# Optimization experiments

Hardware: AMD Instinct MI355X
Metric: run time of the kernel (lower is better)

## Reference

```python
import jax, jax.numpy as jnp
import numpy as np

NUM_HEADING_BIN = 12
NUM_SIZE_CLUSTER = 8
BS = 524288
# KITTI-style mean box sizes (l, w, h) for 8 size clusters
G_MEAN_SIZE_ARR = np.array([
    [3.88, 1.63, 1.53], [0.84, 0.66, 1.76], [1.76, 0.60, 1.74], [16.17, 2.58, 3.23],
    [3.90, 1.60, 1.56], [1.73, 0.58, 1.37], [0.91, 0.48, 1.78], [2.06, 1.86, 1.66]],
    dtype=np.float32)


def setup_inputs() -> dict:
    key = jax.random.key(0)
    ks = jax.random.split(key, 13)
    f = lambda k, s: jax.random.normal(k, s, dtype=jnp.float32)
    return {
        "center": f(ks[0], (BS, 3)),
        "center_label": f(ks[1], (BS, 3)),
        "stage1_center": f(ks[2], (BS, 3)),
        "heading_scores": f(ks[3], (BS, 12)),
        "heading_residuals_normalized": f(ks[4], (BS, 12)),
        "heading_residuals": f(ks[5], (BS, 12)),
        "heading_class_label": jax.random.randint(ks[6], (BS,), 0, 12, dtype=jnp.int64),
        "heading_residuals_label": f(ks[7], (BS,)),
        "size_scores": f(ks[8], (BS, 8)),
        "size_residuals_normalized": f(ks[9], (BS, 8, 3)),
        "size_residuals": f(ks[10], (BS, 8, 3)),
        "size_class_label": jax.random.randint(ks[11], (BS,), 0, 8, dtype=jnp.int64),
        "size_residuals_label": f(ks[12], (BS, 3)),
    }


def _huber(err, delta):
    a = jnp.abs(err)
    q = jnp.minimum(a, delta)
    return jnp.mean(0.5 * q * q + delta * (a - q))


_SX = jnp.array([1, 1, -1, -1, 1, 1, -1, -1], dtype=jnp.float32)
_SY = jnp.array([1, 1, 1, 1, -1, -1, -1, -1], dtype=jnp.float32)
_SZ = jnp.array([1, -1, -1, 1, 1, -1, -1, 1], dtype=jnp.float32)


def _corners3d(centers, headings, sizes):
    # centers (bs,3), headings (bs,), sizes (bs,3) [l,w,h] -> (bs,8,3)
    l, w, h = sizes[:, 0:1], sizes[:, 1:2], sizes[:, 2:3]
    x = 0.5 * l * _SX  # (bs,8)
    y = 0.5 * h * _SY
    z = 0.5 * w * _SZ
    c = jnp.cos(headings)[:, None]
    s = jnp.sin(headings)[:, None]
    xr = c * x + s * z   # rotation about y-axis
    zr = -s * x + c * z
    return jnp.stack([xr, y, zr], axis=-1) + centers[:, None, :]


def reference(center, center_label, stage1_center, heading_scores,
              heading_residuals_normalized, heading_residuals, heading_class_label,
              heading_residuals_label, size_scores, size_residuals_normalized,
              size_residuals, size_class_label, size_residuals_label):
    corner_loss_weight, box_loss_weight = 10.0, 1.0
    mean_sizes = jnp.asarray(G_MEAN_SIZE_ARR)  # (8,3)
    hcls = heading_class_label.astype(jnp.int32)
    scls = size_class_label.astype(jnp.int32)

    center_loss = _huber(jnp.linalg.norm(center - center_label, axis=1), 2.0)
    stage1_center_loss = _huber(jnp.linalg.norm(center - stage1_center, axis=1), 1.0)

    h_logp = jax.nn.log_softmax(heading_scores, axis=1)
    heading_class_loss = -jnp.mean(jnp.take_along_axis(h_logp, hcls[:, None], axis=1))
    s_logp = jax.nn.log_softmax(size_scores, axis=1)
    size_class_loss = -jnp.mean(jnp.take_along_axis(s_logp, scls[:, None], axis=1))

    # heading residual loss (one-hot sum == gather at class index)
    hres_label_norm = heading_residuals_label / (np.pi / NUM_HEADING_BIN)
    hres_pred = jnp.take_along_axis(heading_residuals_normalized, hcls[:, None], axis=1)[:, 0]
    heading_res_loss = _huber(hres_pred - hres_label_norm, 1.0)

    # size residual loss
    sres_pred = jnp.take_along_axis(size_residuals_normalized, scls[:, None, None], axis=1)[:, 0]  # (bs,3)
    mean_size_label = mean_sizes[scls]  # (bs,3)
    sres_label_norm = size_residuals_label / mean_size_label
    size_res_loss = _huber(jnp.linalg.norm(sres_label_norm - sres_pred, axis=1), 1.0)

    # corner loss: gt_mask one-hot sum over (NH,NS) grid == gather (hcls, scls) box
    bin_centers = jnp.arange(NUM_HEADING_BIN, dtype=jnp.float32) * (2.0 * np.pi / NUM_HEADING_BIN)
    heading_pred = jnp.take_along_axis(heading_residuals, hcls[:, None], axis=1)[:, 0] + bin_centers[hcls]
    size_pred = mean_size_label + jnp.take_along_axis(size_residuals, scls[:, None, None], axis=1)[:, 0]
    corners_pred = _corners3d(center, heading_pred, size_pred)  # (bs,8,3)

    heading_label = heading_residuals_label + bin_centers[hcls]
    size_label = mean_size_label + size_residuals_label
    corners_gt = _corners3d(center_label, heading_label, size_label)
    corners_gt_flip = _corners3d(center_label, heading_label + np.pi, size_label)
    corners_dist = jnp.minimum(jnp.linalg.norm(corners_pred - corners_gt, axis=-1),
                               jnp.linalg.norm(corners_pred - corners_gt_flip, axis=-1))
    corners_loss = _huber(corners_dist, 1.0)

    total_loss = box_loss_weight * (center_loss + heading_class_loss + size_class_loss
                                    + heading_res_loss * 20.0 + size_res_loss * 20.0
                                    + stage1_center_loss + corner_loss_weight * corners_loss)
    return total_loss
```

## Files before the change

kernel.cpp:

```cpp
#include <hip/hip_runtime.h>
#include <math.h>


constexpr int BS_N = 524288;
constexpr int NBLK = 4096;

__constant__ float G_MEAN[8][3] = {
    {3.88f, 1.63f, 1.53f}, {0.84f, 0.66f, 1.76f}, {1.76f, 0.60f, 1.74f},
    {16.17f, 2.58f, 3.23f}, {3.90f, 1.60f, 1.56f}, {1.73f, 0.58f, 1.37f},
    {0.91f, 0.48f, 1.78f}, {2.06f, 1.86f, 1.66f}
};
__constant__ float G_RCP[8][3] = {
    {1.0f/3.88f, 1.0f/1.63f, 1.0f/1.53f}, {1.0f/0.84f, 1.0f/0.66f, 1.0f/1.76f},
    {1.0f/1.76f, 1.0f/0.60f, 1.0f/1.74f}, {1.0f/16.17f, 1.0f/2.58f, 1.0f/3.23f},
    {1.0f/3.90f, 1.0f/1.60f, 1.0f/1.56f}, {1.0f/1.73f, 1.0f/0.58f, 1.0f/1.37f},
    {1.0f/0.91f, 1.0f/0.48f, 1.0f/1.78f}, {1.0f/2.06f, 1.0f/1.86f, 1.0f/1.66f}
};

__device__ __forceinline__ float huber_pos(float a, float delta) {
    return (a <= delta) ? 0.5f * a * a : delta * (a - 0.5f * delta);
}
__device__ __forceinline__ float huber_norm2(float d2, float delta) {
    return (d2 <= delta * delta) ? 0.5f * d2
                                 : delta * (sqrtf(d2) - 0.5f * delta);
}
__device__ __forceinline__ float sel4(float4 v, int k) {
    float r = v.x;
    r = (k == 1) ? v.y : r;
    r = (k == 2) ? v.z : r;
    r = (k == 3) ? v.w : r;
    return r;
}
__device__ __forceinline__ float sel12(float4 a, float4 b, float4 c, int k) {
    float r = sel4(a, k);
    r = (k >= 4) ? sel4(b, k - 4) : r;
    r = (k >= 8) ? sel4(c, k - 8) : r;
    return r;
}
__device__ __forceinline__ float sel8(float4 a, float4 b, int k) {
    float r = sel4(a, k);
    r = (k >= 4) ? sel4(b, k - 4) : r;
    return r;
}
__device__ __forceinline__ void sel_row3(
    float4 a, float4 b, float4 c, float4 d, float4 e, float4 f, int s,
    float &o0, float &o1, float &o2)
{
    const float r[24] = {a.x,a.y,a.z,a.w, b.x,b.y,b.z,b.w, c.x,c.y,c.z,c.w,
                         d.x,d.y,d.z,d.w, e.x,e.y,e.z,e.w, f.x,f.y,f.z,f.w};
    o0 = r[0]; o1 = r[1]; o2 = r[2];
    #pragma unroll
    for (int k = 1; k < 8; ++k) {
        const bool m = (s == k);
        o0 = m ? r[3*k+0] : o0;
        o1 = m ? r[3*k+1] : o1;
        o2 = m ? r[3*k+2] : o2;
    }
}

__global__ __launch_bounds__(128) void bbox_partial(
    const float* __restrict__ center,
    const float* __restrict__ center_label,
    const float* __restrict__ stage1_center,
    const float* __restrict__ heading_scores,
    const float* __restrict__ hrn,
    const float* __restrict__ hres,
    const int*   __restrict__ hcls_in,
    const float* __restrict__ hres_label,
    const float* __restrict__ size_scores,
    const float* __restrict__ srn,
    const float* __restrict__ sres,
    const int*   __restrict__ scls_in,
    const float* __restrict__ sres_label,
    float* __restrict__ block_out)
{
    const int i = blockIdx.x * 128 + threadIdx.x;

    const int h = hcls_in[i];
    const int s = scls_in[i];

    const float cx = center[3*i+0], cy = center[3*i+1], cz = center[3*i+2];
    const float lx = center_label[3*i+0], ly = center_label[3*i+1], lz = center_label[3*i+2];
    const float tx = stage1_center[3*i+0], ty = stage1_center[3*i+1], tz = stage1_center[3*i+2];
    const float sl0 = sres_label[3*i+0], sl1 = sres_label[3*i+1], sl2 = sres_label[3*i+2];
    const float hrl = hres_label[i];

    const float4* hsp = reinterpret_cast<const float4*>(heading_scores + 12*i);
    const float4 hsA = hsp[0], hsB = hsp[1], hsC = hsp[2];
    const float4* ssp = reinterpret_cast<const float4*>(size_scores + 8*i);
    const float4 ssA = ssp[0], ssB = ssp[1];

    const float4* hnp = reinterpret_cast<const float4*>(hrn + 12*i);
    const float4 hn0 = hnp[0], hn1 = hnp[1], hn2 = hnp[2];
    const float4* hep = reinterpret_cast<const float4*>(hres + 12*i);
    const float4 he0 = hep[0], he1 = hep[1], he2 = hep[2];

    const float4* snp = reinterpret_cast<const float4*>(srn + 24*i);
    const float4 sn0 = snp[0], sn1 = snp[1], sn2 = snp[2],
                 sn3 = snp[3], sn4 = snp[4], sn5 = snp[5];
    const float4* srp = reinterpret_cast<const float4*>(sres + 24*i);
    const float4 sr0 = srp[0], sr1 = srp[1], sr2 = srp[2],
                 sr3 = srp[3], sr4 = srp[4], sr5 = srp[5];

    float contrib = 0.0f;

    const float dx0 = cx - lx, dy0 = cy - ly, dz0 = cz - lz;
    contrib += huber_norm2(dx0*dx0 + dy0*dy0 + dz0*dz0, 2.0f);
    {
        const float ax = cx - tx, ay = cy - ty, az = cz - tz;
        contrib += huber_norm2(ax*ax + ay*ay + az*az, 1.0f);
    }

    {
        float m = fmaxf(fmaxf(fmaxf(hsA.x,hsA.y),fmaxf(hsA.z,hsA.w)),
                  fmaxf(fmaxf(fmaxf(hsB.x,hsB.y),fmaxf(hsB.z,hsB.w)),
                        fmaxf(fmaxf(hsC.x,hsC.y),fmaxf(hsC.z,hsC.w))));
        float se = __expf(hsA.x-m)+__expf(hsA.y-m)+__expf(hsA.z-m)+__expf(hsA.w-m)
                 + __expf(hsB.x-m)+__expf(hsB.y-m)+__expf(hsB.z-m)+__expf(hsB.w-m)
                 + __expf(hsC.x-m)+__expf(hsC.y-m)+__expf(hsC.z-m)+__expf(hsC.w-m);
        contrib += m + __logf(se) - sel12(hsA, hsB, hsC, h);
    }
    {
        float m = fmaxf(fmaxf(fmaxf(ssA.x,ssA.y),fmaxf(ssA.z,ssA.w)),
                        fmaxf(fmaxf(ssB.x,ssB.y),fmaxf(ssB.z,ssB.w)));
        float se = __expf(ssA.x-m)+__expf(ssA.y-m)+__expf(ssA.z-m)+__expf(ssA.w-m)
                 + __expf(ssB.x-m)+__expf(ssB.y-m)+__expf(ssB.z-m)+__expf(ssB.w-m);
        contrib += m + __logf(se) - sel8(ssA, ssB, s);
    }

    const float hrnv = sel12(hn0, hn1, hn2, h);
    const float hrev = sel12(he0, he1, he2, h);
    float snv0, snv1, snv2, srv0, srv1, srv2;
    sel_row3(sn0, sn1, sn2, sn3, sn4, sn5, s, snv0, snv1, snv2);
    sel_row3(sr0, sr1, sr2, sr3, sr4, sr5, s, srv0, srv1, srv2);

    contrib += 20.0f * huber_pos(fabsf(hrnv - hrl * (float)(12.0 / M_PI)), 1.0f);

    const float m0 = G_MEAN[s][0], m1 = G_MEAN[s][1], m2c = G_MEAN[s][2];
    {
        const float e0 = sl0 * G_RCP[s][0] - snv0;
        const float e1 = sl1 * G_RCP[s][1] - snv1;
        const float e2 = sl2 * G_RCP[s][2] - snv2;
        contrib += 20.0f * huber_norm2(e0*e0 + e1*e1 + e2*e2, 1.0f);
    }

    {
        const float binc = (float)h * (float)(M_PI / 6.0);
        const float hp = hrev + binc;
        const float hg = hrl + binc;
        const float lp2 = 0.5f * (m0 + srv0);
        const float wp2 = 0.5f * (m1 + srv1);
        const float hp2 = 0.5f * (m2c + srv2);
        const float lg2 = 0.5f * (m0 + sl0);
        const float wg2 = 0.5f * (m1 + sl1);
        const float hg2 = 0.5f * (m2c + sl2);
        float cp, sp, cg, sg;
        __sincosf(hp, &sp, &cp);
        __sincosf(hg, &sg, &cg);
        const float dyh = hp2 - hg2;

        constexpr float SX[8] = {1,1,-1,-1,1,1,-1,-1};
        constexpr float SY[8] = {1,1,1,1,-1,-1,-1,-1};
        constexpr float SZ[8] = {1,-1,-1,1,1,-1,-1,1};
        float csum = 0.0f;
        #pragma unroll
        for (int j = 0; j < 8; ++j) {
            const float axp = SX[j]*lp2, azp = SZ[j]*wp2;
            const float xrp = cp*axp + sp*azp;
            const float zrp = cp*azp - sp*axp;
            const float axg = SX[j]*lg2, azg = SZ[j]*wg2;
            const float xrg = cg*axg + sg*azg;
            const float zrg = cg*azg - sg*axg;
            const float ddy = dy0 + SY[j]*dyh;
            const float u = dx0 + xrp, v = dz0 + zrp;
            const float du1 = u - xrg, dv1 = v - zrg;
            const float du2 = u + xrg, dv2 = v + zrg;
            const float y2 = ddy*ddy;
            const float dgt = du1*du1 + y2 + dv1*dv1;
            const float dfl = du2*du2 + y2 + dv2*dv2;
            const float mm = fminf(dgt, dfl);
            csum += (mm <= 1.0f) ? 0.5f*mm : sqrtf(mm) - 0.5f;
        }
        contrib += 1.25f * csum;
    }

    #pragma unroll
    for (int off = 32; off > 0; off >>= 1)
        contrib += __shfl_down(contrib, off, 64);

    __shared__ float sdata[2];
    const int lane = threadIdx.x & 63;
    const int wid  = threadIdx.x >> 6;
    if (lane == 0) sdata[wid] = contrib;
    __syncthreads();
    if (threadIdx.x == 0)
        block_out[blockIdx.x] = sdata[0] + sdata[1];
}

__global__ __launch_bounds__(256) void bbox_final(
    const float* __restrict__ block_in, float* __restrict__ out)
{
    float ssum = 0.0f;
    for (int i = threadIdx.x; i < NBLK; i += 256)
        ssum += block_in[i];
    #pragma unroll
    for (int off = 32; off > 0; off >>= 1)
        ssum += __shfl_down(ssum, off, 64);

    __shared__ float sdata[4];
    const int lane = threadIdx.x & 63;
    const int wid  = threadIdx.x >> 6;
    if (lane == 0) sdata[wid] = ssum;
    __syncthreads();
    if (threadIdx.x == 0)
        out[0] = ((sdata[0] + sdata[1]) + (sdata[2] + sdata[3])) * (1.0f / (float)BS_N);
}

extern "C" void kernel_launch(void* const* d_in, const int* in_sizes, int n_in,
                              void* d_out, int out_size, void* d_ws, size_t ws_size,
                              hipStream_t stream) {
    const float* center        = (const float*)d_in[0];
    const float* center_label  = (const float*)d_in[1];
    const float* stage1_center = (const float*)d_in[2];
    const float* heading_sc    = (const float*)d_in[3];
    const float* hrn           = (const float*)d_in[4];
    const float* hres          = (const float*)d_in[5];
    const int*   hcls          = (const int*)d_in[6];
    const float* hres_label    = (const float*)d_in[7];
    const float* size_sc       = (const float*)d_in[8];
    const float* srn           = (const float*)d_in[9];
    const float* sres          = (const float*)d_in[10];
    const int*   scls          = (const int*)d_in[11];
    const float* sres_label    = (const float*)d_in[12];

    float* ws  = (float*)d_ws;
    float* out = (float*)d_out;

    bbox_partial<<<NBLK, 128, 0, stream>>>(
        center, center_label, stage1_center, heading_sc, hrn, hres,
        hcls, hres_label, size_sc, srn, sres, scls, sres_label, ws);
    bbox_final<<<1, 256, 0, stream>>>(ws, out);
}
```

Before: 42.57 us.

## Gather selected residuals directly and fuse final reduction via last-block atomic

Instead of loading all 12 heading residuals and all 24 size residuals per row and selecting in registers, the kernel now gathers only the entries picked by the class labels. This cuts DRAM traffic for four large arrays, at the cost of scattered, poorly coalesced reads. The separate final reduction kernel is replaced by a last-block-done pattern using an atomic counter, which adds a memset launch. The block size doubles to 256.

```diff
diff --git a/kernel.cpp b/kernel.cpp
--- a/kernel.cpp
+++ b/kernel.cpp
@@ -3,7 +3,7 @@
 
 
 constexpr int BS_N = 524288;
-constexpr int NBLK = 4096;
+constexpr int NBLK = 2048;
 
 __constant__ float G_MEAN[8][3] = {
     {3.88f, 1.63f, 1.53f}, {0.84f, 0.66f, 1.76f}, {1.76f, 0.60f, 1.74f},
@@ -42,23 +42,8 @@
     r = (k >= 4) ? sel4(b, k - 4) : r;
     return r;
 }
-__device__ __forceinline__ void sel_row3(
-    float4 a, float4 b, float4 c, float4 d, float4 e, float4 f, int s,
-    float &o0, float &o1, float &o2)
-{
-    const float r[24] = {a.x,a.y,a.z,a.w, b.x,b.y,b.z,b.w, c.x,c.y,c.z,c.w,
-                         d.x,d.y,d.z,d.w, e.x,e.y,e.z,e.w, f.x,f.y,f.z,f.w};
-    o0 = r[0]; o1 = r[1]; o2 = r[2];
-    #pragma unroll
-    for (int k = 1; k < 8; ++k) {
-        const bool m = (s == k);
-        o0 = m ? r[3*k+0] : o0;
-        o1 = m ? r[3*k+1] : o1;
-        o2 = m ? r[3*k+2] : o2;
-    }
-}
-
-__global__ __launch_bounds__(128) void bbox_partial(
+
+__global__ __launch_bounds__(256) void bbox_fused(
     const float* __restrict__ center,
     const float* __restrict__ center_label,
     const float* __restrict__ stage1_center,
@@ -72,9 +57,11 @@
     const float* __restrict__ sres,
     const int*   __restrict__ scls_in,
     const float* __restrict__ sres_label,
-    float* __restrict__ block_out)
+    float* __restrict__ partials,
+    unsigned int* __restrict__ counter,
+    float* __restrict__ out)
 {
-    const int i = blockIdx.x * 128 + threadIdx.x;
+    const int i = blockIdx.x * 256 + threadIdx.x;
 
     const int h = hcls_in[i];
     const int s = scls_in[i];
@@ -90,17 +77,11 @@
     const float4* ssp = reinterpret_cast<const float4*>(size_scores + 8*i);
     const float4 ssA = ssp[0], ssB = ssp[1];
 
-    const float4* hnp = reinterpret_cast<const float4*>(hrn + 12*i);
-    const float4 hn0 = hnp[0], hn1 = hnp[1], hn2 = hnp[2];
-    const float4* hep = reinterpret_cast<const float4*>(hres + 12*i);
-    const float4 he0 = hep[0], he1 = hep[1], he2 = hep[2];
-
-    const float4* snp = reinterpret_cast<const float4*>(srn + 24*i);
-    const float4 sn0 = snp[0], sn1 = snp[1], sn2 = snp[2],
-                 sn3 = snp[3], sn4 = snp[4], sn5 = snp[5];
-    const float4* srp = reinterpret_cast<const float4*>(sres + 24*i);
-    const float4 sr0 = srp[0], sr1 = srp[1], sr2 = srp[2],
-                 sr3 = srp[3], sr4 = srp[4], sr5 = srp[5];
+    const float hrnv = hrn [12*i + h];
+    const float hrev = hres[12*i + h];
+    const int   sb   = (8*i + s) * 3;
+    const float snv0 = srn [sb+0], snv1 = srn [sb+1], snv2 = srn [sb+2];
+    const float srv0 = sres[sb+0], srv1 = sres[sb+1], srv2 = sres[sb+2];
 
     float contrib = 0.0f;
 
@@ -127,12 +108,6 @@
                  + __expf(ssB.x-m)+__expf(ssB.y-m)+__expf(ssB.z-m)+__expf(ssB.w-m);
         contrib += m + __logf(se) - sel8(ssA, ssB, s);
     }
-
-    const float hrnv = sel12(hn0, hn1, hn2, h);
-    const float hrev = sel12(he0, he1, he2, h);
-    float snv0, snv1, snv2, srv0, srv1, srv2;
-    sel_row3(sn0, sn1, sn2, sn3, sn4, sn5, s, snv0, snv1, snv2);
-    sel_row3(sr0, sr1, sr2, sr3, sr4, sr5, s, srv0, srv1, srv2);
 
     contrib += 20.0f * huber_pos(fabsf(hrnv - hrl * (float)(12.0 / M_PI)), 1.0f);
 
@@ -188,32 +163,36 @@
     for (int off = 32; off > 0; off >>= 1)
         contrib += __shfl_down(contrib, off, 64);
 
-    __shared__ float sdata[2];
+    __shared__ float sdata[4];
+    __shared__ int islast;
     const int lane = threadIdx.x & 63;
     const int wid  = threadIdx.x >> 6;
     if (lane == 0) sdata[wid] = contrib;
     __syncthreads();
-    if (threadIdx.x == 0)
-        block_out[blockIdx.x] = sdata[0] + sdata[1];
-}
-
-__global__ __launch_bounds__(256) void bbox_final(
-    const float* __restrict__ block_in, float* __restrict__ out)
-{
+    if (threadIdx.x == 0) {
+        const float bsum = (sdata[0] + sdata[1]) + (sdata[2] + sdata[3]);
+        __hip_atomic_store(&partials[blockIdx.x], bsum,
+                           __ATOMIC_RELEASE, __HIP_MEMORY_SCOPE_AGENT);
+        const unsigned t = __hip_atomic_fetch_add(counter, 1u,
+                           __ATOMIC_ACQ_REL, __HIP_MEMORY_SCOPE_AGENT);
+        islast = (t == (unsigned)(NBLK - 1));
+    }
+    __syncthreads();
+    if (!islast) return;
+
     float ssum = 0.0f;
-    for (int i = threadIdx.x; i < NBLK; i += 256)
-        ssum += block_in[i];
+    #pragma unroll
+    for (int k = 0; k < NBLK / 256; ++k)
+        ssum += __hip_atomic_load(&partials[threadIdx.x + 256 * k],
+                                  __ATOMIC_RELAXED, __HIP_MEMORY_SCOPE_AGENT);
     #pragma unroll
     for (int off = 32; off > 0; off >>= 1)
         ssum += __shfl_down(ssum, off, 64);
-
-    __shared__ float sdata[4];
-    const int lane = threadIdx.x & 63;
-    const int wid  = threadIdx.x >> 6;
     if (lane == 0) sdata[wid] = ssum;
     __syncthreads();
     if (threadIdx.x == 0)
-        out[0] = ((sdata[0] + sdata[1]) + (sdata[2] + sdata[3])) * (1.0f / (float)BS_N);
+        out[0] = ((sdata[0] + sdata[1]) + (sdata[2] + sdata[3]))
+                 * (1.0f / (float)BS_N);
 }
 
 extern "C" void kernel_launch(void* const* d_in, const int* in_sizes, int n_in,
@@ -233,11 +212,14 @@
     const int*   scls          = (const int*)d_in[11];
     const float* sres_label    = (const float*)d_in[12];
 
-    float* ws  = (float*)d_ws;
-    float* out = (float*)d_out;
-
-    bbox_partial<<<NBLK, 128, 0, stream>>>(
+    float*        partials = (float*)d_ws;
+    unsigned int* counter  = (unsigned int*)((char*)d_ws + NBLK * sizeof(float));
+    float*        out      = (float*)d_out;
+
+    hipMemsetAsync(counter, 0, sizeof(unsigned int), stream);
+
+    bbox_fused<<<NBLK, 256, 0, stream>>>(
         center, center_label, stage1_center, heading_sc, hrn, hres,
-        hcls, hres_label, size_sc, srn, sres, scls, sres_label, ws);
-    bbox_final<<<1, 256, 0, stream>>>(ws, out);
-}
+        hcls, hres_label, size_sc, srn, sres, scls, sres_label,
+        partials, counter, out);
+}
```

New measurement: 153.7 us. 3.61x slower.
